# Kernel optimization log

Measured on AMD Instinct MI355X. Metric: run time of the kernel, lower is better.

## Reference

```python
import jax, jax.numpy as jnp
import numpy as np

H, DK, NW = 16, 8, 8   # num_heads, d_k (== n_wires_attn), n_wires_ffn
EPS = 1e-5


def _ln(x, g, b):
    mu = jnp.mean(x, axis=-1, keepdims=True)
    v = jnp.mean((x - mu) ** 2, axis=-1, keepdims=True)
    return (x - mu) / jnp.sqrt(v + EPS) * g + b


def setup_inputs() -> dict:
    key = jax.random.key(0)
    ks = jax.random.split(key, 10)
    B, S, E, F = 4, 1024, 128, 512

    def lin(k, o, i):
        lim = 1.0 / np.sqrt(i)
        k1, k2 = jax.random.split(k)
        W = jax.random.uniform(k1, (o, i), minval=-lim, maxval=lim, dtype=jnp.float32)
        b = jax.random.uniform(k2, (o,), minval=-lim, maxval=lim, dtype=jnp.float32)
        return W, b

    Wq, bq = lin(ks[0], E, E)
    Wk, bk = lin(ks[1], E, E)
    Wv, bv = lin(ks[2], E, E)
    Wo, bo = lin(ks[3], E, E)
    W1, b1 = lin(ks[4], F, NW)
    W2, b2 = lin(ks[5], E, F)
    rx_params = jax.random.uniform(ks[6], (H, DK), minval=0.0, maxval=2.0 * np.pi, dtype=jnp.float32)
    ry_params = jax.random.uniform(ks[7], (NW,), minval=0.0, maxval=2.0 * np.pi, dtype=jnp.float32)
    x = jax.random.normal(ks[8], (B, S, E), dtype=jnp.float32)
    return dict(x=x, Wq=Wq, bq=bq, Wk=Wk, bk=bk, Wv=Wv, bv=bv,
                rx_params=rx_params, Wo=Wo, bo=bo, ry_params=ry_params,
                W1=W1, b1=b1, W2=W2, b2=b2,
                ln1_g=jnp.ones((E,), jnp.float32), ln1_b=jnp.zeros((E,), jnp.float32),
                ln2_g=jnp.ones((E,), jnp.float32), ln2_b=jnp.zeros((E,), jnp.float32))


def reference(x, Wq, bq, Wk, bk, Wv, bv, rx_params, Wo, bo, ry_params,
              W1, b1, W2, b2, ln1_g, ln1_b, ln2_g, ln2_b):
    B, S, E = x.shape
    # q projection; k/v are computed in the original but never used downstream
    q = (x @ Wq.T + bq).reshape(B, S, H, DK).transpose(0, 2, 1, 3)  # [B,H,S,dk]
    # per-head single-qubit circuit RX(phi)RX(q)|0> -> <Z> = cos(q + phi)
    out = jnp.cos(q + rx_params[None, :, None, :])                  # [B,H,S,dk]
    scores = jnp.einsum('bhsd,bhtd->bhst', out, out) / np.sqrt(DK)  # [B,H,S,S]
    attn = jax.nn.softmax(scores, axis=-1)
    ctx = jnp.einsum('bhst,bhtd->bhsd', attn, out)
    ctx = ctx.transpose(0, 2, 1, 3).reshape(B, S, E)
    x1 = _ln(x + ctx @ Wo.T + bo, ln1_g, ln1_b)
    # FFN circuit RY(phi)RX(x)|0> -> <Z> = cos(x)*cos(phi); only first NW feats used
    qout = jnp.cos(x1[..., :NW]) * jnp.cos(ry_params)               # [B,S,NW]
    ffn = jax.nn.relu(qout @ W1.T + b1) @ W2.T + b2
    return _ln(x1 + ffn, ln2_g, ln2_b)
```

## Files before the change

### kernel.cpp

```cpp
#include <hip/hip_runtime.h>
#include <math.h>

constexpr int B_ = 4, S_ = 1024, E_ = 128, H_ = 16, DK_ = 8, F_ = 512;
constexpr int R_ = B_ * S_;
#define EPSV 1e-5f

constexpr int OFF_WQT  = 0;
constexpr int OFF_WOT  = OFF_WQT + E_ * E_;
constexpr int OFF_W2T  = OFF_WOT + E_ * E_;
constexpr int OFF_QCB  = OFF_W2T + F_ * E_;
constexpr int OFF_VTB  = OFF_QCB + 262144;
constexpr int OFF_X1   = OFF_QCB;
constexpr int OFF_CTX  = OFF_VTB + 262144;
constexpr int OFF_QOUT = OFF_CTX + R_ * E_;

typedef __attribute__((ext_vector_type(4)))  short short4v;
typedef __attribute__((ext_vector_type(16))) float f32x16;

static __device__ __forceinline__ void fma4(float4& acc, float s, const float4 v) {
    acc.x = fmaf(s, v.x, acc.x);
    acc.y = fmaf(s, v.y, acc.y);
    acc.z = fmaf(s, v.z, acc.z);
    acc.w = fmaf(s, v.w, acc.w);
}

static __device__ __forceinline__ short4v pack2(unsigned a, unsigned b) {
    union { unsigned u[2]; short4v s; } t;
    t.u[0] = a; t.u[1] = b;
    return t.s;
}

static __device__ __forceinline__ short4v cvt4_bf16(float a, float b, float c, float d) {
    unsigned p0, p1;
    asm("v_cvt_pk_bf16_f32 %0, %1, %2" : "=v"(p0) : "v"(a), "v"(b));
    asm("v_cvt_pk_bf16_f32 %0, %1, %2" : "=v"(p1) : "v"(c), "v"(d));
    return pack2(p0, p1);
}

__global__ __launch_bounds__(256) void k_transpose(const float* __restrict__ Wq,
                                                   const float* __restrict__ Wo,
                                                   const float* __restrict__ W2,
                                                   float* __restrict__ ws) {
    int idx = blockIdx.x * 256 + threadIdx.x;
    if (idx < 16384) {
        int e = idx >> 7, k = idx & 127;
        ws[OFF_WQT + k * 128 + e] = Wq[idx];
    } else if (idx < 32768) {
        int j = idx - 16384;
        int e = j >> 7, k = j & 127;
        ws[OFF_WOT + k * 128 + e] = Wo[j];
    } else if (idx < 98304) {
        int j = idx - 32768;
        int e = j >> 9, f = j & 511;
        ws[OFF_W2T + f * 128 + e] = W2[j];
    }
}

__global__ __launch_bounds__(256) void k_qproj(const float* __restrict__ x,
                                               const float* __restrict__ bq,
                                               const float* __restrict__ rx,
                                               const float* __restrict__ WqT,
                                               short* __restrict__ qcb,
                                               short* __restrict__ vtb) {
    __shared__ __attribute__((aligned(16))) float xs[8][128];
    const int tid = threadIdx.x;
    const int row0 = blockIdx.x * 8;
    ((float4*)xs)[tid] = ((const float4*)(x + row0 * E_))[tid];
    __syncthreads();
    const int cg = tid & 31, rs = tid >> 5;
    const int c0 = cg * 4;
    const float* wp = WqT + c0;
    float4 acc = {0.f, 0.f, 0.f, 0.f};
#pragma unroll 4
    for (int k0 = 0; k0 < 128; k0 += 4) {
        const float4 u  = *(const float4*)&xs[rs][k0];
        const float4 w0 = *(const float4*)(wp + (k0 + 0) * 128);
        const float4 w1 = *(const float4*)(wp + (k0 + 1) * 128);
        const float4 w2 = *(const float4*)(wp + (k0 + 2) * 128);
        const float4 w3 = *(const float4*)(wp + (k0 + 3) * 128);
        fma4(acc, u.x, w0);
        fma4(acc, u.y, w1);
        fma4(acc, u.z, w2);
        fma4(acc, u.w, w3);
    }
    const float4 bb = *(const float4*)(bq + c0);
    const float4 rr = *(const float4*)(rx + c0);
    const int gr = row0 + rs;
    const int b = gr >> 10, s = gr & 1023;
    const int h = c0 >> 3, d0 = c0 & 7;
    const int bh = b * H_ + h;
    float4 o;
    o.x = cosf(acc.x + bb.x + rr.x);
    o.y = cosf(acc.y + bb.y + rr.y);
    o.z = cosf(acc.z + bb.z + rr.z);
    o.w = cosf(acc.w + bb.w + rr.w);
    const short4v q4 = cvt4_bf16(o.x, o.y, o.z, o.w);
    *(short4v*)(qcb + (size_t)(bh * S_ + s) * 8 + d0) = q4;
    vtb[(bh * 8 + d0 + 0) * S_ + s] = q4[0];
    vtb[(bh * 8 + d0 + 1) * S_ + s] = q4[1];
    vtb[(bh * 8 + d0 + 2) * S_ + s] = q4[2];
    vtb[(bh * 8 + d0 + 3) * S_ + s] = q4[3];
}

__global__ __launch_bounds__(256) void k_attn(const short* __restrict__ qcb,
                                              const short* __restrict__ vtb,
                                              float* __restrict__ ctx) {
    constexpr float SC = 0.35355339059327373f;
    const int tid = threadIdx.x;
    const int bh = blockIdx.x >> 3;
    const int qt = blockIdx.x & 7;
    const int lane = tid & 63;
    const int row = lane & 31, hi = lane >> 5;
    const int q0 = qt * 128 + (tid >> 6) * 32;

    const short4v qfrag = *(const short4v*)(qcb + (size_t)(bh * S_ + q0 + row) * 8 + 4 * hi);
    const short* kb = qcb + (size_t)bh * S_ * 8 + 4 * hi;
    const bool vok = row < 8;
    const short* vb = vtb + (size_t)(bh * 8 + (row & 7)) * S_ + 4 * hi;
    const short4v zf = {0, 0, 0, 0};

    f32x16 pacc = {0,0,0,0,0,0,0,0,0,0,0,0,0,0,0,0};
    const f32x16 zacc = {0,0,0,0,0,0,0,0,0,0,0,0,0,0,0,0};
    float lsum = 0.f;

#pragma unroll 2
    for (int tk = 0; tk < S_; tk += 32) {
        const short4v kfrag = *(const short4v*)(kb + (size_t)(tk + row) * 8);
        f32x16 sd = __builtin_amdgcn_mfma_f32_32x32x8bf16_1k(kfrag, qfrag, zacc, 0, 0, 0);

        short4v pb0, pb1, pb2, pb3;
#define PCHUNK(c, pbv) { \
        const float e0 = __expf(sd[4*(c)+0] * SC); \
        const float e1 = __expf(sd[4*(c)+1] * SC); \
        const float e2 = __expf(sd[4*(c)+2] * SC); \
        const float e3 = __expf(sd[4*(c)+3] * SC); \
        lsum += (e0 + e1) + (e2 + e3); \
        pbv = cvt4_bf16(e0, e1, e2, e3); }
        PCHUNK(0, pb0)
        PCHUNK(1, pb1)
        PCHUNK(2, pb2)
        PCHUNK(3, pb3)
#undef PCHUNK

        const short4v v0 = vok ? *(const short4v*)(vb + tk +  0) : zf;
        const short4v v1 = vok ? *(const short4v*)(vb + tk +  8) : zf;
        const short4v v2 = vok ? *(const short4v*)(vb + tk + 16) : zf;
        const short4v v3 = vok ? *(const short4v*)(vb + tk + 24) : zf;
        pacc = __builtin_amdgcn_mfma_f32_32x32x8bf16_1k(v0, pb0, pacc, 0, 0, 0);
        pacc = __builtin_amdgcn_mfma_f32_32x32x8bf16_1k(v1, pb1, pacc, 0, 0, 0);
        pacc = __builtin_amdgcn_mfma_f32_32x32x8bf16_1k(v2, pb2, pacc, 0, 0, 0);
        pacc = __builtin_amdgcn_mfma_f32_32x32x8bf16_1k(v3, pb3, pacc, 0, 0, 0);
    }

    lsum += __shfl_xor(lsum, 32);
    const float inv = 1.0f / lsum;
    const int b = bh >> 4, h = bh & 15;
    float4 o;
    o.x = pacc[0] * inv; o.y = pacc[1] * inv;
    o.z = pacc[2] * inv; o.w = pacc[3] * inv;
    *(float4*)(ctx + (size_t)(b * S_ + q0 + row) * E_ + h * 8 + 4 * hi) = o;
}

__global__ __launch_bounds__(256) void k_oproj_ln1(const float* __restrict__ ctx,
                                                   const float* __restrict__ WoT,
                                                   const float* __restrict__ bo,
                                                   const float* __restrict__ x,
                                                   const float* __restrict__ g1,
                                                   const float* __restrict__ bln1,
                                                   const float* __restrict__ ry,
                                                   float* __restrict__ x1,
                                                   float* __restrict__ qout) {
    __shared__ __attribute__((aligned(16))) float cs[8][128];
    const int tid = threadIdx.x;
    const int row0 = blockIdx.x * 8;
    ((float4*)cs)[tid] = ((const float4*)(ctx + row0 * E_))[tid];
    __syncthreads();
    const int cg = tid & 31, rs = tid >> 5;
    const int c0 = cg * 4;
    const float* wp = WoT + c0;
    float4 acc = {0.f, 0.f, 0.f, 0.f};
#pragma unroll 4
    for (int k0 = 0; k0 < 128; k0 += 4) {
        const float4 u  = *(const float4*)&cs[rs][k0];
        const float4 w0 = *(const float4*)(wp + (k0 + 0) * 128);
        const float4 w1 = *(const float4*)(wp + (k0 + 1) * 128);
        const float4 w2 = *(const float4*)(wp + (k0 + 2) * 128);
        const float4 w3 = *(const float4*)(wp + (k0 + 3) * 128);
        fma4(acc, u.x, w0);
        fma4(acc, u.y, w1);
        fma4(acc, u.z, w2);
        fma4(acc, u.w, w3);
    }
    const int gr = row0 + rs;
    const float4 bb = *(const float4*)(bo + c0);
    const float4 xx = *(const float4*)(x + gr * E_ + c0);
    float4 y;
    y.x = acc.x + bb.x + xx.x;
    y.y = acc.y + bb.y + xx.y;
    y.z = acc.z + bb.z + xx.z;
    y.w = acc.w + bb.w + xx.w;
    float s = (y.x + y.y) + (y.z + y.w);
    float q = fmaf(y.x, y.x, y.y * y.y) + fmaf(y.z, y.z, y.w * y.w);
#pragma unroll
    for (int m = 1; m < 32; m <<= 1) {
        s += __shfl_xor(s, m);
        q += __shfl_xor(q, m);
    }
    const float mu = s * (1.0f / 128.0f);
    const float var = q * (1.0f / 128.0f) - mu * mu;
    const float is = rsqrtf(var + EPSV);
    const float4 gg = *(const float4*)(g1 + c0);
    const float4 lb = *(const float4*)(bln1 + c0);
    float4 o;
    o.x = (y.x - mu) * is * gg.x + lb.x;
    o.y = (y.y - mu) * is * gg.y + lb.y;
    o.z = (y.z - mu) * is * gg.z + lb.z;
    o.w = (y.w - mu) * is * gg.w + lb.w;
    *(float4*)(x1 + gr * E_ + c0) = o;
    if (c0 < 8) {
        float4 qo;
        qo.x = cosf(o.x) * cosf(ry[c0 + 0]);
        qo.y = cosf(o.y) * cosf(ry[c0 + 1]);
        qo.z = cosf(o.z) * cosf(ry[c0 + 2]);
        qo.w = cosf(o.w) * cosf(ry[c0 + 3]);
        *(float4*)(qout + gr * 8 + c0) = qo;
    }
}

__global__ __launch_bounds__(256) void k_ffn_ln2(const float* __restrict__ qout,
                                                 const float* __restrict__ W1,
                                                 const float* __restrict__ b1,
                                                 const float* __restrict__ W2T,
                                                 const float* __restrict__ b2,
                                                 const float* __restrict__ x1,
                                                 const float* __restrict__ g2,
                                                 const float* __restrict__ bln2,
                                                 float* __restrict__ out) {
    __shared__ __attribute__((aligned(16))) float qs[8][8];
    __shared__ __attribute__((aligned(16))) float h1[8][512];
    const int tid = threadIdx.x;
    const int row0 = blockIdx.x * 8;
    if (tid < 16) ((float4*)qs)[tid] = ((const float4*)(qout + row0 * 8))[tid];
    __syncthreads();
#pragma unroll
    for (int i = 0; i < 16; ++i) {
        const int f = ((i & 1) << 8) + tid;
        const int r = i >> 1;
        const float4 wa = *(const float4*)(W1 + f * 8);
        const float4 wb = *(const float4*)(W1 + f * 8 + 4);
        float v = b1[f];
        v = fmaf(qs[r][0], wa.x, v); v = fmaf(qs[r][1], wa.y, v);
        v = fmaf(qs[r][2], wa.z, v); v = fmaf(qs[r][3], wa.w, v);
        v = fmaf(qs[r][4], wb.x, v); v = fmaf(qs[r][5], wb.y, v);
        v = fmaf(qs[r][6], wb.z, v); v = fmaf(qs[r][7], wb.w, v);
        h1[r][f] = fmaxf(v, 0.0f);
    }
    __syncthreads();
    const int cg = tid & 31, rs = tid >> 5;
    const int c0 = cg * 4;
    const float* wp = W2T + c0;
    float4 acc = {0.f, 0.f, 0.f, 0.f};
#pragma unroll 4
    for (int f0 = 0; f0 < 512; f0 += 4) {
        const float4 u  = *(const float4*)&h1[rs][f0];
        const float4 w0 = *(const float4*)(wp + (f0 + 0) * 128);
        const float4 w1 = *(const float4*)(wp + (f0 + 1) * 128);
        const float4 w2 = *(const float4*)(wp + (f0 + 2) * 128);
        const float4 w3 = *(const float4*)(wp + (f0 + 3) * 128);
        fma4(acc, u.x, w0);
        fma4(acc, u.y, w1);
        fma4(acc, u.z, w2);
        fma4(acc, u.w, w3);
    }
    const int gr = row0 + rs;
    const float4 bb = *(const float4*)(b2 + c0);
    const float4 xx = *(const float4*)(x1 + gr * E_ + c0);
    float4 y;
    y.x = acc.x + bb.x + xx.x;
    y.y = acc.y + bb.y + xx.y;
    y.z = acc.z + bb.z + xx.z;
    y.w = acc.w + bb.w + xx.w;
    float s = (y.x + y.y) + (y.z + y.w);
    float q = fmaf(y.x, y.x, y.y * y.y) + fmaf(y.z, y.z, y.w * y.w);
#pragma unroll
    for (int m = 1; m < 32; m <<= 1) {
        s += __shfl_xor(s, m);
        q += __shfl_xor(q, m);
    }
    const float mu = s * (1.0f / 128.0f);
    const float var = q * (1.0f / 128.0f) - mu * mu;
    const float is = rsqrtf(var + EPSV);
    const float4 gg = *(const float4*)(g2 + c0);
    const float4 lb = *(const float4*)(bln2 + c0);
    float4 o;
    o.x = (y.x - mu) * is * gg.x + lb.x;
    o.y = (y.y - mu) * is * gg.y + lb.y;
    o.z = (y.z - mu) * is * gg.z + lb.z;
    o.w = (y.w - mu) * is * gg.w + lb.w;
    *(float4*)(out + gr * E_ + c0) = o;
}

extern "C" void kernel_launch(void* const* d_in, const int* in_sizes, int n_in,
                              void* d_out, int out_size, void* d_ws, size_t ws_size,
                              hipStream_t stream) {
    const float* x   = (const float*)d_in[0];
    const float* Wq  = (const float*)d_in[1];
    const float* bq  = (const float*)d_in[2];
    const float* rx  = (const float*)d_in[7];
    const float* Wo  = (const float*)d_in[8];
    const float* bo  = (const float*)d_in[9];
    const float* ry  = (const float*)d_in[10];
    const float* W1  = (const float*)d_in[11];
    const float* b1  = (const float*)d_in[12];
    const float* W2  = (const float*)d_in[13];
    const float* b2  = (const float*)d_in[14];
    const float* g1  = (const float*)d_in[15];
    const float* bl1 = (const float*)d_in[16];
    const float* g2  = (const float*)d_in[17];
    const float* bl2 = (const float*)d_in[18];
    float* ws  = (float*)d_ws;
    float* out = (float*)d_out;
    short* qcb = (short*)(ws + OFF_QCB);
    short* vtb = (short*)(ws + OFF_VTB);

    k_transpose<<<dim3(384), dim3(256), 0, stream>>>(Wq, Wo, W2, ws);
    k_qproj<<<dim3(R_ / 8), dim3(256), 0, stream>>>(x, bq, rx, ws + OFF_WQT, qcb, vtb);
    k_attn<<<dim3(B_ * H_ * 8), dim3(256), 0, stream>>>(qcb, vtb, ws + OFF_CTX);
    k_oproj_ln1<<<dim3(R_ / 8), dim3(256), 0, stream>>>(ws + OFF_CTX, ws + OFF_WOT, bo, x,
                                                        g1, bl1, ry,
                                                        ws + OFF_X1, ws + OFF_QOUT);
    k_ffn_ln2<<<dim3(R_ / 8), dim3(256), 0, stream>>>(ws + OFF_QOUT, W1, b1, ws + OFF_W2T,
                                                      b2, ws + OFF_X1, g2, bl2, out);
}
```

Baseline: 181.2 us.

## Process two rows per thread, stage V transpose in LDS, tile weight transpose

The projection, o-proj+LN1 and FFN+LN2 kernels now handle 16 rows per block, with each thread computing two rows. This reuses every weight float4 load across two accumulators and halves the block count. The q-projection stages the transposed V tile in shared memory, so vtb is written with 16-byte coalesced stores instead of scattered 2-byte stores. The weight transpose kernel uses a 32x32 padded LDS tile with float4 loads and stores. The trade-off is higher register use and fewer blocks, which could lower occupancy on a GPU this size.

```diff
diff --git a/kernel.cpp b/kernel.cpp
--- a/kernel.cpp
+++ b/kernel.cpp
@@ -15,6 +15,7 @@
 constexpr int OFF_QOUT = OFF_CTX + R_ * E_;
 
 typedef __attribute__((ext_vector_type(4)))  short short4v;
+typedef __attribute__((ext_vector_type(8)))  short short8v;
 typedef __attribute__((ext_vector_type(16))) float f32x16;
 
 static __device__ __forceinline__ void fma4(float4& acc, float s, const float4 v) {
@@ -41,19 +42,24 @@
                                                    const float* __restrict__ Wo,
                                                    const float* __restrict__ W2,
                                                    float* __restrict__ ws) {
-    int idx = blockIdx.x * 256 + threadIdx.x;
-    if (idx < 16384) {
-        int e = idx >> 7, k = idx & 127;
-        ws[OFF_WQT + k * 128 + e] = Wq[idx];
-    } else if (idx < 32768) {
-        int j = idx - 16384;
-        int e = j >> 7, k = j & 127;
-        ws[OFF_WOT + k * 128 + e] = Wo[j];
-    } else if (idx < 98304) {
-        int j = idx - 32768;
-        int e = j >> 9, f = j & 511;
-        ws[OFF_W2T + f * 128 + e] = W2[j];
-    }
+    __shared__ float ts[32][33];
+    const int t = blockIdx.x, tid = threadIdx.x;
+    const float* src; float* dst; int lds_, ldd, r0s, c0s;
+    if (t < 16)      { src = Wq; dst = ws + OFF_WQT; lds_ = 128; ldd = 128;
+                       r0s = (t & 3) * 32;        c0s = (t >> 2) * 32; }
+    else if (t < 32) { int u = t - 16; src = Wo; dst = ws + OFF_WOT; lds_ = 128; ldd = 128;
+                       r0s = (u & 3) * 32;        c0s = (u >> 2) * 32; }
+    else             { int u = t - 32; src = W2; dst = ws + OFF_W2T; lds_ = 512; ldd = 128;
+                       r0s = (u & 3) * 32;        c0s = (u >> 2) * 32; }
+    const int rr = tid >> 3, cc = (tid & 7) * 4;
+    const float4 v = *(const float4*)(src + (r0s + rr) * lds_ + c0s + cc);
+    ts[rr][cc + 0] = v.x; ts[rr][cc + 1] = v.y;
+    ts[rr][cc + 2] = v.z; ts[rr][cc + 3] = v.w;
+    __syncthreads();
+    float4 o;
+    o.x = ts[cc + 0][rr]; o.y = ts[cc + 1][rr];
+    o.z = ts[cc + 2][rr]; o.w = ts[cc + 3][rr];
+    *(float4*)(dst + (c0s + rr) * ldd + r0s + cc) = o;
 }
 
 __global__ __launch_bounds__(256) void k_qproj(const float* __restrict__ x,
@@ -62,44 +68,57 @@
                                                const float* __restrict__ WqT,
                                                short* __restrict__ qcb,
                                                short* __restrict__ vtb) {
-    __shared__ __attribute__((aligned(16))) float xs[8][128];
+    __shared__ __attribute__((aligned(16))) float xs[16][128];
+    __shared__ __attribute__((aligned(16))) short vts[128][20];
     const int tid = threadIdx.x;
-    const int row0 = blockIdx.x * 8;
-    ((float4*)xs)[tid] = ((const float4*)(x + row0 * E_))[tid];
-    __syncthreads();
-    const int cg = tid & 31, rs = tid >> 5;
-    const int c0 = cg * 4;
+    const int row0 = blockIdx.x * 16;
+    {
+        const float4* src = (const float4*)(x + row0 * E_);
+        ((float4*)xs)[tid]       = src[tid];
+        ((float4*)xs)[tid + 256] = src[tid + 256];
+    }
+    __syncthreads();
+    const int cg = tid & 31, rg = tid >> 5;
+    const int c0 = cg * 4, r0 = rg * 2;
     const float* wp = WqT + c0;
-    float4 acc = {0.f, 0.f, 0.f, 0.f};
+    float4 a0 = {0.f,0.f,0.f,0.f}, a1 = {0.f,0.f,0.f,0.f};
 #pragma unroll 4
     for (int k0 = 0; k0 < 128; k0 += 4) {
-        const float4 u  = *(const float4*)&xs[rs][k0];
         const float4 w0 = *(const float4*)(wp + (k0 + 0) * 128);
         const float4 w1 = *(const float4*)(wp + (k0 + 1) * 128);
         const float4 w2 = *(const float4*)(wp + (k0 + 2) * 128);
         const float4 w3 = *(const float4*)(wp + (k0 + 3) * 128);
-        fma4(acc, u.x, w0);
-        fma4(acc, u.y, w1);
-        fma4(acc, u.z, w2);
-        fma4(acc, u.w, w3);
+        const float4 u0 = *(const float4*)&xs[r0][k0];
+        const float4 u1 = *(const float4*)&xs[r0 + 1][k0];
+        fma4(a0, u0.x, w0); fma4(a1, u1.x, w0);
+        fma4(a0, u0.y, w1); fma4(a1, u1.y, w1);
+        fma4(a0, u0.z, w2); fma4(a1, u1.z, w2);
+        fma4(a0, u0.w, w3); fma4(a1, u1.w, w3);
     }
     const float4 bb = *(const float4*)(bq + c0);
     const float4 rr = *(const float4*)(rx + c0);
-    const int gr = row0 + rs;
-    const int b = gr >> 10, s = gr & 1023;
+    const int b = row0 >> 10, sB = row0 & 1023;
     const int h = c0 >> 3, d0 = c0 & 7;
     const int bh = b * H_ + h;
-    float4 o;
-    o.x = cosf(acc.x + bb.x + rr.x);
-    o.y = cosf(acc.y + bb.y + rr.y);
-    o.z = cosf(acc.z + bb.z + rr.z);
-    o.w = cosf(acc.w + bb.w + rr.w);
-    const short4v q4 = cvt4_bf16(o.x, o.y, o.z, o.w);
-    *(short4v*)(qcb + (size_t)(bh * S_ + s) * 8 + d0) = q4;
-    vtb[(bh * 8 + d0 + 0) * S_ + s] = q4[0];
-    vtb[(bh * 8 + d0 + 1) * S_ + s] = q4[1];
-    vtb[(bh * 8 + d0 + 2) * S_ + s] = q4[2];
-    vtb[(bh * 8 + d0 + 3) * S_ + s] = q4[3];
+    float4 o0, o1;
+    o0.x = cosf(a0.x + bb.x + rr.x); o0.y = cosf(a0.y + bb.y + rr.y);
+    o0.z = cosf(a0.z + bb.z + rr.z); o0.w = cosf(a0.w + bb.w + rr.w);
+    o1.x = cosf(a1.x + bb.x + rr.x); o1.y = cosf(a1.y + bb.y + rr.y);
+    o1.z = cosf(a1.z + bb.z + rr.z); o1.w = cosf(a1.w + bb.w + rr.w);
+    const short4v q0 = cvt4_bf16(o0.x, o0.y, o0.z, o0.w);
+    const short4v q1 = cvt4_bf16(o1.x, o1.y, o1.z, o1.w);
+    *(short4v*)(qcb + (size_t)(bh * S_ + sB + r0) * 8 + d0)     = q0;
+    *(short4v*)(qcb + (size_t)(bh * S_ + sB + r0 + 1) * 8 + d0) = q1;
+    vts[c0 + 0][r0] = q0[0]; vts[c0 + 1][r0] = q0[1];
+    vts[c0 + 2][r0] = q0[2]; vts[c0 + 3][r0] = q0[3];
+    vts[c0 + 0][r0 + 1] = q1[0]; vts[c0 + 1][r0 + 1] = q1[1];
+    vts[c0 + 2][r0 + 1] = q1[2]; vts[c0 + 3][r0 + 1] = q1[3];
+    __syncthreads();
+    const int e = tid >> 1, hf = tid & 1;
+    short8v vv;
+#pragma unroll
+    for (int j = 0; j < 8; ++j) vv[j] = vts[e][hf * 8 + j];
+    *(short8v*)(vtb + (size_t)(b * 128 + e) * S_ + sB + hf * 8) = vv;
 }
 
 __global__ __launch_bounds__(256) void k_attn(const short* __restrict__ qcb,
@@ -170,60 +189,79 @@
                                                    const float* __restrict__ ry,
                                                    float* __restrict__ x1,
                                                    float* __restrict__ qout) {
-    __shared__ __attribute__((aligned(16))) float cs[8][128];
+    __shared__ __attribute__((aligned(16))) float cs[16][128];
     const int tid = threadIdx.x;
-    const int row0 = blockIdx.x * 8;
-    ((float4*)cs)[tid] = ((const float4*)(ctx + row0 * E_))[tid];
-    __syncthreads();
-    const int cg = tid & 31, rs = tid >> 5;
-    const int c0 = cg * 4;
+    const int row0 = blockIdx.x * 16;
+    {
+        const float4* src = (const float4*)(ctx + row0 * E_);
+        ((float4*)cs)[tid]       = src[tid];
+        ((float4*)cs)[tid + 256] = src[tid + 256];
+    }
+    __syncthreads();
+    const int cg = tid & 31, rg = tid >> 5;
+    const int c0 = cg * 4, r0 = rg * 2;
     const float* wp = WoT + c0;
-    float4 acc = {0.f, 0.f, 0.f, 0.f};
+    float4 a0 = {0.f,0.f,0.f,0.f}, a1 = {0.f,0.f,0.f,0.f};
 #pragma unroll 4
     for (int k0 = 0; k0 < 128; k0 += 4) {
-        const float4 u  = *(const float4*)&cs[rs][k0];
         const float4 w0 = *(const float4*)(wp + (k0 + 0) * 128);
         const float4 w1 = *(const float4*)(wp + (k0 + 1) * 128);
         const float4 w2 = *(const float4*)(wp + (k0 + 2) * 128);
         const float4 w3 = *(const float4*)(wp + (k0 + 3) * 128);
-        fma4(acc, u.x, w0);
-        fma4(acc, u.y, w1);
-        fma4(acc, u.z, w2);
-        fma4(acc, u.w, w3);
-    }
-    const int gr = row0 + rs;
+        const float4 u0 = *(const float4*)&cs[r0][k0];
+        const float4 u1 = *(const float4*)&cs[r0 + 1][k0];
+        fma4(a0, u0.x, w0); fma4(a1, u1.x, w0);
+        fma4(a0, u0.y, w1); fma4(a1, u1.y, w1);
+        fma4(a0, u0.z, w2); fma4(a1, u1.z, w2);
+        fma4(a0, u0.w, w3); fma4(a1, u1.w, w3);
+    }
+    const int gr0 = row0 + r0, gr1 = gr0 + 1;
     const float4 bb = *(const float4*)(bo + c0);
-    const float4 xx = *(const float4*)(x + gr * E_ + c0);
-    float4 y;
-    y.x = acc.x + bb.x + xx.x;
-    y.y = acc.y + bb.y + xx.y;
-    y.z = acc.z + bb.z + xx.z;
-    y.w = acc.w + bb.w + xx.w;
-    float s = (y.x + y.y) + (y.z + y.w);
-    float q = fmaf(y.x, y.x, y.y * y.y) + fmaf(y.z, y.z, y.w * y.w);
+    const float4 xa = *(const float4*)(x + gr0 * E_ + c0);
+    const float4 xb = *(const float4*)(x + gr1 * E_ + c0);
+    float4 y0, y1;
+    y0.x = a0.x + bb.x + xa.x; y0.y = a0.y + bb.y + xa.y;
+    y0.z = a0.z + bb.z + xa.z; y0.w = a0.w + bb.w + xa.w;
+    y1.x = a1.x + bb.x + xb.x; y1.y = a1.y + bb.y + xb.y;
+    y1.z = a1.z + bb.z + xb.z; y1.w = a1.w + bb.w + xb.w;
+    float s0 = (y0.x + y0.y) + (y0.z + y0.w);
+    float q0 = fmaf(y0.x, y0.x, y0.y * y0.y) + fmaf(y0.z, y0.z, y0.w * y0.w);
+    float s1 = (y1.x + y1.y) + (y1.z + y1.w);
+    float q1 = fmaf(y1.x, y1.x, y1.y * y1.y) + fmaf(y1.z, y1.z, y1.w * y1.w);
 #pragma unroll
     for (int m = 1; m < 32; m <<= 1) {
-        s += __shfl_xor(s, m);
-        q += __shfl_xor(q, m);
-    }
-    const float mu = s * (1.0f / 128.0f);
-    const float var = q * (1.0f / 128.0f) - mu * mu;
-    const float is = rsqrtf(var + EPSV);
+        s0 += __shfl_xor(s0, m); q0 += __shfl_xor(q0, m);
+        s1 += __shfl_xor(s1, m); q1 += __shfl_xor(q1, m);
+    }
+    const float mu0 = s0 * (1.0f / 128.0f);
+    const float is0 = rsqrtf(q0 * (1.0f / 128.0f) - mu0 * mu0 + EPSV);
+    const float mu1 = s1 * (1.0f / 128.0f);
+    const float is1 = rsqrtf(q1 * (1.0f / 128.0f) - mu1 * mu1 + EPSV);
     const float4 gg = *(const float4*)(g1 + c0);
     const float4 lb = *(const float4*)(bln1 + c0);
-    float4 o;
-    o.x = (y.x - mu) * is * gg.x + lb.x;
-    o.y = (y.y - mu) * is * gg.y + lb.y;
-    o.z = (y.z - mu) * is * gg.z + lb.z;
-    o.w = (y.w - mu) * is * gg.w + lb.w;
-    *(float4*)(x1 + gr * E_ + c0) = o;
+    float4 o0, o1;
+    o0.x = (y0.x - mu0) * is0 * gg.x + lb.x;
+    o0.y = (y0.y - mu0) * is0 * gg.y + lb.y;
+    o0.z = (y0.z - mu0) * is0 * gg.z + lb.z;
+    o0.w = (y0.w - mu0) * is0 * gg.w + lb.w;
+    o1.x = (y1.x - mu1) * is1 * gg.x + lb.x;
+    o1.y = (y1.y - mu1) * is1 * gg.y + lb.y;
+    o1.z = (y1.z - mu1) * is1 * gg.z + lb.z;
+    o1.w = (y1.w - mu1) * is1 * gg.w + lb.w;
+    *(float4*)(x1 + gr0 * E_ + c0) = o0;
+    *(float4*)(x1 + gr1 * E_ + c0) = o1;
     if (c0 < 8) {
-        float4 qo;
-        qo.x = cosf(o.x) * cosf(ry[c0 + 0]);
-        qo.y = cosf(o.y) * cosf(ry[c0 + 1]);
-        qo.z = cosf(o.z) * cosf(ry[c0 + 2]);
-        qo.w = cosf(o.w) * cosf(ry[c0 + 3]);
-        *(float4*)(qout + gr * 8 + c0) = qo;
+        float4 qo0, qo1;
+        qo0.x = cosf(o0.x) * cosf(ry[c0 + 0]);
+        qo0.y = cosf(o0.y) * cosf(ry[c0 + 1]);
+        qo0.z = cosf(o0.z) * cosf(ry[c0 + 2]);
+        qo0.w = cosf(o0.w) * cosf(ry[c0 + 3]);
+        qo1.x = cosf(o1.x) * cosf(ry[c0 + 0]);
+        qo1.y = cosf(o1.y) * cosf(ry[c0 + 1]);
+        qo1.z = cosf(o1.z) * cosf(ry[c0 + 2]);
+        qo1.w = cosf(o1.w) * cosf(ry[c0 + 3]);
+        *(float4*)(qout + gr0 * 8 + c0) = qo0;
+        *(float4*)(qout + gr1 * 8 + c0) = qo1;
     }
 }
 
@@ -236,14 +274,14 @@
                                                  const float* __restrict__ g2,
                                                  const float* __restrict__ bln2,
                                                  float* __restrict__ out) {
-    __shared__ __attribute__((aligned(16))) float qs[8][8];
-    __shared__ __attribute__((aligned(16))) float h1[8][512];
+    __shared__ __attribute__((aligned(16))) float qs[16][8];
+    __shared__ __attribute__((aligned(16))) float h1[16][512];
     const int tid = threadIdx.x;
-    const int row0 = blockIdx.x * 8;
-    if (tid < 16) ((float4*)qs)[tid] = ((const float4*)(qout + row0 * 8))[tid];
+    const int row0 = blockIdx.x * 16;
+    if (tid < 32) ((float4*)qs)[tid] = ((const float4*)(qout + row0 * 8))[tid];
     __syncthreads();
 #pragma unroll
-    for (int i = 0; i < 16; ++i) {
+    for (int i = 0; i < 32; ++i) {
         const int f = ((i & 1) << 8) + tid;
         const int r = i >> 1;
         const float4 wa = *(const float4*)(W1 + f * 8);
@@ -256,48 +294,58 @@
         h1[r][f] = fmaxf(v, 0.0f);
     }
     __syncthreads();
-    const int cg = tid & 31, rs = tid >> 5;
-    const int c0 = cg * 4;
+    const int cg = tid & 31, rg = tid >> 5;
+    const int c0 = cg * 4, r0 = rg * 2;
     const float* wp = W2T + c0;
-    float4 acc = {0.f, 0.f, 0.f, 0.f};
+    float4 a0 = {0.f,0.f,0.f,0.f}, a1 = {0.f,0.f,0.f,0.f};
 #pragma unroll 4
     for (int f0 = 0; f0 < 512; f0 += 4) {
-        const float4 u  = *(const float4*)&h1[rs][f0];
         const float4 w0 = *(const float4*)(wp + (f0 + 0) * 128);
         const float4 w1 = *(const float4*)(wp + (f0 + 1) * 128);
         const float4 w2 = *(const float4*)(wp + (f0 + 2) * 128);
         const float4 w3 = *(const float4*)(wp + (f0 + 3) * 128);
-        fma4(acc, u.x, w0);
-        fma4(acc, u.y, w1);
-        fma4(acc, u.z, w2);
-        fma4(acc, u.w, w3);
-    }
-    const int gr = row0 + rs;
+        const float4 u0 = *(const float4*)&h1[r0][f0];
+        const float4 u1 = *(const float4*)&h1[r0 + 1][f0];
+        fma4(a0, u0.x, w0); fma4(a1, u1.x, w0);
+        fma4(a0, u0.y, w1); fma4(a1, u1.y, w1);
+        fma4(a0, u0.z, w2); fma4(a1, u1.z, w2);
+        fma4(a0, u0.w, w3); fma4(a1, u1.w, w3);
+    }
+    const int gr0 = row0 + r0, gr1 = gr0 + 1;
     const float4 bb = *(const float4*)(b2 + c0);
-    const float4 xx = *(const float4*)(x1 + gr * E_ + c0);
-    float4 y;
-    y.x = acc.x + bb.x + xx.x;
-    y.y = acc.y + bb.y + xx.y;
-    y.z = acc.z + bb.z + xx.z;
-    y.w = acc.w + bb.w + xx.w;
-    float s = (y.x + y.y) + (y.z + y.w);
-    float q = fmaf(y.x, y.x, y.y * y.y) + fmaf(y.z, y.z, y.w * y.w);
+    const float4 xa = *(const float4*)(x1 + gr0 * E_ + c0);
+    const float4 xb = *(const float4*)(x1 + gr1 * E_ + c0);
+    float4 y0, y1;
+    y0.x = a0.x + bb.x + xa.x; y0.y = a0.y + bb.y + xa.y;
+    y0.z = a0.z + bb.z + xa.z; y0.w = a0.w + bb.w + xa.w;
+    y1.x = a1.x + bb.x + xb.x; y1.y = a1.y + bb.y + xb.y;
+    y1.z = a1.z + bb.z + xb.z; y1.w = a1.w + bb.w + xb.w;
+    float s0 = (y0.x + y0.y) + (y0.z + y0.w);
+    float q0 = fmaf(y0.x, y0.x, y0.y * y0.y) + fmaf(y0.z, y0.z, y0.w * y0.w);
+    float s1 = (y1.x + y1.y) + (y1.z + y1.w);
+    float q1 = fmaf(y1.x, y1.x, y1.y * y1.y) + fmaf(y1.z, y1.z, y1.w * y1.w);
 #pragma unroll
     for (int m = 1; m < 32; m <<= 1) {
-        s += __shfl_xor(s, m);
-        q += __shfl_xor(q, m);
-    }
-    const float mu = s * (1.0f / 128.0f);
-    const float var = q * (1.0f / 128.0f) - mu * mu;
-    const float is = rsqrtf(var + EPSV);
+        s0 += __shfl_xor(s0, m); q0 += __shfl_xor(q0, m);
+        s1 += __shfl_xor(s1, m); q1 += __shfl_xor(q1, m);
+    }
+    const float mu0 = s0 * (1.0f / 128.0f);
+    const float is0 = rsqrtf(q0 * (1.0f / 128.0f) - mu0 * mu0 + EPSV);
+    const float mu1 = s1 * (1.0f / 128.0f);
+    const float is1 = rsqrtf(q1 * (1.0f / 128.0f) - mu1 * mu1 + EPSV);
     const float4 gg = *(const float4*)(g2 + c0);
     const float4 lb = *(const float4*)(bln2 + c0);
-    float4 o;
-    o.x = (y.x - mu) * is * gg.x + lb.x;
-    o.y = (y.y - mu) * is * gg.y + lb.y;
-    o.z = (y.z - mu) * is * gg.z + lb.z;
-    o.w = (y.w - mu) * is * gg.w + lb.w;
-    *(float4*)(out + gr * E_ + c0) = o;
+    float4 o0, o1;
+    o0.x = (y0.x - mu0) * is0 * gg.x + lb.x;
+    o0.y = (y0.y - mu0) * is0 * gg.y + lb.y;
+    o0.z = (y0.z - mu0) * is0 * gg.z + lb.z;
+    o0.w = (y0.w - mu0) * is0 * gg.w + lb.w;
+    o1.x = (y1.x - mu1) * is1 * gg.x + lb.x;
+    o1.y = (y1.y - mu1) * is1 * gg.y + lb.y;
+    o1.z = (y1.z - mu1) * is1 * gg.z + lb.z;
+    o1.w = (y1.w - mu1) * is1 * gg.w + lb.w;
+    *(float4*)(out + gr0 * E_ + c0) = o0;
+    *(float4*)(out + gr1 * E_ + c0) = o1;
 }
 
 extern "C" void kernel_launch(void* const* d_in, const int* in_sizes, int n_in,
@@ -323,12 +371,12 @@
     short* qcb = (short*)(ws + OFF_QCB);
     short* vtb = (short*)(ws + OFF_VTB);
 
-    k_transpose<<<dim3(384), dim3(256), 0, stream>>>(Wq, Wo, W2, ws);
-    k_qproj<<<dim3(R_ / 8), dim3(256), 0, stream>>>(x, bq, rx, ws + OFF_WQT, qcb, vtb);
+    k_transpose<<<dim3(96), dim3(256), 0, stream>>>(Wq, Wo, W2, ws);
+    k_qproj<<<dim3(R_ / 16), dim3(256), 0, stream>>>(x, bq, rx, ws + OFF_WQT, qcb, vtb);
     k_attn<<<dim3(B_ * H_ * 8), dim3(256), 0, stream>>>(qcb, vtb, ws + OFF_CTX);
-    k_oproj_ln1<<<dim3(R_ / 8), dim3(256), 0, stream>>>(ws + OFF_CTX, ws + OFF_WOT, bo, x,
-                                                        g1, bl1, ry,
-                                                        ws + OFF_X1, ws + OFF_QOUT);
-    k_ffn_ln2<<<dim3(R_ / 8), dim3(256), 0, stream>>>(ws + OFF_QOUT, W1, b1, ws + OFF_W2T,
-                                                      b2, ws + OFF_X1, g2, bl2, out);
-}
+    k_oproj_ln1<<<dim3(R_ / 16), dim3(256), 0, stream>>>(ws + OFF_CTX, ws + OFF_WOT, bo, x,
+                                                         g1, bl1, ry,
+                                                         ws + OFF_X1, ws + OFF_QOUT);
+    k_ffn_ln2<<<dim3(R_ / 16), dim3(256), 0, stream>>>(ws + OFF_QOUT, W1, b1, ws + OFF_W2T,
+                                                       b2, ws + OFF_X1, g2, bl2, out);
+}
```

After: 188.4 us. 4.0% more time.

## Move projections and FFN GEMMs to bf16 MFMA with bf16 intermediates

Applied to the files above, without the earlier changes.

Replaces the scalar fp32 FMA GEMMs in the q-projection, output projection and FFN kernels with 32x32x8 bf16 MFMA tiles over 32-row blocks. A new prep kernel converts x and the weights to bf16 instead of transposing them. Intermediates (ctx, x1, qout) are now stored as bf16, and LayerNorm is redone through a shared-memory transpose. This cuts FMA work and memory traffic at the cost of lower precision in the residual x1 and the GEMM inputs.

```diff
diff --git a/kernel.cpp b/kernel.cpp
--- a/kernel.cpp
+++ b/kernel.cpp
@@ -5,24 +5,20 @@
 constexpr int R_ = B_ * S_;
 #define EPSV 1e-5f
 
-constexpr int OFF_WQT  = 0;
-constexpr int OFF_WOT  = OFF_WQT + E_ * E_;
-constexpr int OFF_W2T  = OFF_WOT + E_ * E_;
-constexpr int OFF_QCB  = OFF_W2T + F_ * E_;
-constexpr int OFF_VTB  = OFF_QCB + 262144;
-constexpr int OFF_X1   = OFF_QCB;
-constexpr int OFF_CTX  = OFF_VTB + 262144;
-constexpr int OFF_QOUT = OFF_CTX + R_ * E_;
+constexpr size_t OFF_XB   = 0;
+constexpr size_t OFF_WQB  = OFF_XB   + 524288;
+constexpr size_t OFF_WOB  = OFF_WQB  + 16384;
+constexpr size_t OFF_W1B  = OFF_WOB  + 16384;
+constexpr size_t OFF_W2B  = OFF_W1B  + 4096;
+constexpr size_t OFF_QCB  = OFF_W2B  + 65536;
+constexpr size_t OFF_VTB  = OFF_QCB  + 524288;
+constexpr size_t OFF_CTXB = OFF_VTB  + 524288;
+constexpr size_t OFF_X1B  = OFF_CTXB + 524288;
+constexpr size_t OFF_QOB  = OFF_X1B  + 524288;
 
 typedef __attribute__((ext_vector_type(4)))  short short4v;
+typedef __attribute__((ext_vector_type(8)))  short short8v;
 typedef __attribute__((ext_vector_type(16))) float f32x16;
-
-static __device__ __forceinline__ void fma4(float4& acc, float s, const float4 v) {
-    acc.x = fmaf(s, v.x, acc.x);
-    acc.y = fmaf(s, v.y, acc.y);
-    acc.z = fmaf(s, v.z, acc.z);
-    acc.w = fmaf(s, v.w, acc.w);
-}
 
 static __device__ __forceinline__ short4v pack2(unsigned a, unsigned b) {
     union { unsigned u[2]; short4v s; } t;
@@ -37,74 +33,79 @@
     return pack2(p0, p1);
 }
 
-__global__ __launch_bounds__(256) void k_transpose(const float* __restrict__ Wq,
-                                                   const float* __restrict__ Wo,
-                                                   const float* __restrict__ W2,
-                                                   float* __restrict__ ws) {
-    int idx = blockIdx.x * 256 + threadIdx.x;
-    if (idx < 16384) {
-        int e = idx >> 7, k = idx & 127;
-        ws[OFF_WQT + k * 128 + e] = Wq[idx];
-    } else if (idx < 32768) {
-        int j = idx - 16384;
-        int e = j >> 7, k = j & 127;
-        ws[OFF_WOT + k * 128 + e] = Wo[j];
-    } else if (idx < 98304) {
-        int j = idx - 32768;
-        int e = j >> 9, f = j & 511;
-        ws[OFF_W2T + f * 128 + e] = W2[j];
-    }
-}
-
-__global__ __launch_bounds__(256) void k_qproj(const float* __restrict__ x,
+static __device__ __forceinline__ short8v cvt8_bf16(const float* v) {
+    const short4v a = cvt4_bf16(v[0], v[1], v[2], v[3]);
+    const short4v b = cvt4_bf16(v[4], v[5], v[6], v[7]);
+    short8v r;
+    r[0]=a[0]; r[1]=a[1]; r[2]=a[2]; r[3]=a[3];
+    r[4]=b[0]; r[5]=b[1]; r[6]=b[2]; r[7]=b[3];
+    return r;
+}
+
+static __device__ __forceinline__ float b2f(short v) {
+    return __uint_as_float(((unsigned)(unsigned short)v) << 16);
+}
+
+__global__ __launch_bounds__(256) void k_prep(const float* __restrict__ x,
+                                              const float* __restrict__ Wq,
+                                              const float* __restrict__ Wo,
+                                              const float* __restrict__ W1,
+                                              const float* __restrict__ W2,
+                                              short* __restrict__ ws) {
+    const int idx = blockIdx.x * 256 + threadIdx.x;
+    const float* src; short* dst; int local;
+    if (idx < 131072)      { src = x;  dst = ws + OFF_XB;  local = idx; }
+    else if (idx < 135168) { src = Wq; dst = ws + OFF_WQB; local = idx - 131072; }
+    else if (idx < 139264) { src = Wo; dst = ws + OFF_WOB; local = idx - 135168; }
+    else if (idx < 140288) { src = W1; dst = ws + OFF_W1B; local = idx - 139264; }
+    else                   { src = W2; dst = ws + OFF_W2B; local = idx - 140288; }
+    const float4 v = ((const float4*)src)[local];
+    ((short4v*)dst)[local] = cvt4_bf16(v.x, v.y, v.z, v.w);
+}
+
+__global__ __launch_bounds__(256) void k_qproj(const short* __restrict__ xb,
                                                const float* __restrict__ bq,
                                                const float* __restrict__ rx,
-                                               const float* __restrict__ WqT,
+                                               const short* __restrict__ wqb,
                                                short* __restrict__ qcb,
                                                short* __restrict__ vtb) {
-    __shared__ __attribute__((aligned(16))) float xs[8][128];
-    const int tid = threadIdx.x;
-    const int row0 = blockIdx.x * 8;
-    ((float4*)xs)[tid] = ((const float4*)(x + row0 * E_))[tid];
-    __syncthreads();
-    const int cg = tid & 31, rs = tid >> 5;
-    const int c0 = cg * 4;
-    const float* wp = WqT + c0;
-    float4 acc = {0.f, 0.f, 0.f, 0.f};
-#pragma unroll 4
-    for (int k0 = 0; k0 < 128; k0 += 4) {
-        const float4 u  = *(const float4*)&xs[rs][k0];
-        const float4 w0 = *(const float4*)(wp + (k0 + 0) * 128);
-        const float4 w1 = *(const float4*)(wp + (k0 + 1) * 128);
-        const float4 w2 = *(const float4*)(wp + (k0 + 2) * 128);
-        const float4 w3 = *(const float4*)(wp + (k0 + 3) * 128);
-        fma4(acc, u.x, w0);
-        fma4(acc, u.y, w1);
-        fma4(acc, u.z, w2);
-        fma4(acc, u.w, w3);
-    }
-    const float4 bb = *(const float4*)(bq + c0);
-    const float4 rr = *(const float4*)(rx + c0);
-    const int gr = row0 + rs;
-    const int b = gr >> 10, s = gr & 1023;
-    const int h = c0 >> 3, d0 = c0 & 7;
+    const int tid = threadIdx.x, lane = tid & 63, w = tid >> 6;
+    const int row = lane & 31, hi = lane >> 5;
+    const int r0 = blockIdx.x * 32;
+    const int c  = w * 32 + row;
+    const short* ap = xb  + (size_t)(r0 + row) * 128 + 4 * hi;
+    const short* bp = wqb + (size_t)c * 128 + 4 * hi;
+    f32x16 acc = {0,0,0,0,0,0,0,0,0,0,0,0,0,0,0,0};
+#pragma unroll
+    for (int k0 = 0; k0 < 128; k0 += 8) {
+        const short4v af = *(const short4v*)(ap + k0);
+        const short4v bf = *(const short4v*)(bp + k0);
+        acc = __builtin_amdgcn_mfma_f32_32x32x8bf16_1k(af, bf, acc, 0, 0, 0);
+    }
+    const float add = bq[c] + rx[c];
+    float cv[16];
+#pragma unroll
+    for (int i = 0; i < 16; ++i) cv[i] = cosf(acc[i] + add);
+    const int b = r0 >> 10, sloc0 = r0 & 1023;
+    const int h = c >> 3, d = c & 7;
     const int bh = b * H_ + h;
-    float4 o;
-    o.x = cosf(acc.x + bb.x + rr.x);
-    o.y = cosf(acc.y + bb.y + rr.y);
-    o.z = cosf(acc.z + bb.z + rr.z);
-    o.w = cosf(acc.w + bb.w + rr.w);
-    const short4v q4 = cvt4_bf16(o.x, o.y, o.z, o.w);
-    *(short4v*)(qcb + (size_t)(bh * S_ + s) * 8 + d0) = q4;
-    vtb[(bh * 8 + d0 + 0) * S_ + s] = q4[0];
-    vtb[(bh * 8 + d0 + 1) * S_ + s] = q4[1];
-    vtb[(bh * 8 + d0 + 2) * S_ + s] = q4[2];
-    vtb[(bh * 8 + d0 + 3) * S_ + s] = q4[3];
+    short* qbase = qcb + ((size_t)bh * 1024 + sloc0) * 8 + d;
+    short* vbase = vtb + ((size_t)bh * 8 + d) * 1024 + sloc0;
+#pragma unroll
+    for (int rq = 0; rq < 4; ++rq) {
+        const short4v v = cvt4_bf16(cv[4*rq+0], cv[4*rq+1], cv[4*rq+2], cv[4*rq+3]);
+        const int sb = 8 * rq + 4 * hi;
+        *(short4v*)(vbase + sb) = v;
+        qbase[(sb + 0) * 8] = v[0];
+        qbase[(sb + 1) * 8] = v[1];
+        qbase[(sb + 2) * 8] = v[2];
+        qbase[(sb + 3) * 8] = v[3];
+    }
 }
 
 __global__ __launch_bounds__(256) void k_attn(const short* __restrict__ qcb,
                                               const short* __restrict__ vtb,
-                                              float* __restrict__ ctx) {
+                                              short* __restrict__ ctxb) {
     constexpr float SC = 0.35355339059327373f;
     const int tid = threadIdx.x;
     const int bh = blockIdx.x >> 3;
@@ -155,149 +156,148 @@
     lsum += __shfl_xor(lsum, 32);
     const float inv = 1.0f / lsum;
     const int b = bh >> 4, h = bh & 15;
-    float4 o;
-    o.x = pacc[0] * inv; o.y = pacc[1] * inv;
-    o.z = pacc[2] * inv; o.w = pacc[3] * inv;
-    *(float4*)(ctx + (size_t)(b * S_ + q0 + row) * E_ + h * 8 + 4 * hi) = o;
-}
-
-__global__ __launch_bounds__(256) void k_oproj_ln1(const float* __restrict__ ctx,
-                                                   const float* __restrict__ WoT,
+    const short4v co = cvt4_bf16(pacc[0] * inv, pacc[1] * inv,
+                                 pacc[2] * inv, pacc[3] * inv);
+    *(short4v*)(ctxb + (size_t)(b * S_ + q0 + row) * 128 + h * 8 + 4 * hi) = co;
+}
+
+__global__ __launch_bounds__(256) void k_oproj_ln1(const short* __restrict__ ctxb,
+                                                   const short* __restrict__ wob,
                                                    const float* __restrict__ bo,
                                                    const float* __restrict__ x,
                                                    const float* __restrict__ g1,
                                                    const float* __restrict__ bln1,
                                                    const float* __restrict__ ry,
-                                                   float* __restrict__ x1,
-                                                   float* __restrict__ qout) {
-    __shared__ __attribute__((aligned(16))) float cs[8][128];
-    const int tid = threadIdx.x;
-    const int row0 = blockIdx.x * 8;
-    ((float4*)cs)[tid] = ((const float4*)(ctx + row0 * E_))[tid];
+                                                   short* __restrict__ x1b,
+                                                   short* __restrict__ qob) {
+    __shared__ float yt[32][129];
+    const int tid = threadIdx.x, lane = tid & 63, w = tid >> 6;
+    const int row = lane & 31, hi = lane >> 5;
+    const int r0 = blockIdx.x * 32;
+    const int c  = w * 32 + row;
+    const short* ap = ctxb + (size_t)(r0 + row) * 128 + 4 * hi;
+    const short* bp = wob  + (size_t)c * 128 + 4 * hi;
+    f32x16 acc = {0,0,0,0,0,0,0,0,0,0,0,0,0,0,0,0};
+#pragma unroll
+    for (int k0 = 0; k0 < 128; k0 += 8) {
+        const short4v af = *(const short4v*)(ap + k0);
+        const short4v bf = *(const short4v*)(bp + k0);
+        acc = __builtin_amdgcn_mfma_f32_32x32x8bf16_1k(af, bf, acc, 0, 0, 0);
+    }
+    const float bov = bo[c];
+#pragma unroll
+    for (int i = 0; i < 16; ++i) {
+        const int sl = (i & 3) + 8 * (i >> 2) + 4 * hi;
+        yt[sl][c] = acc[i] + bov + x[(size_t)(r0 + sl) * 128 + c];
+    }
     __syncthreads();
-    const int cg = tid & 31, rs = tid >> 5;
-    const int c0 = cg * 4;
-    const float* wp = WoT + c0;
-    float4 acc = {0.f, 0.f, 0.f, 0.f};
-#pragma unroll 4
-    for (int k0 = 0; k0 < 128; k0 += 4) {
-        const float4 u  = *(const float4*)&cs[rs][k0];
-        const float4 w0 = *(const float4*)(wp + (k0 + 0) * 128);
-        const float4 w1 = *(const float4*)(wp + (k0 + 1) * 128);
-        const float4 w2 = *(const float4*)(wp + (k0 + 2) * 128);
-        const float4 w3 = *(const float4*)(wp + (k0 + 3) * 128);
-        fma4(acc, u.x, w0);
-        fma4(acc, u.y, w1);
-        fma4(acc, u.z, w2);
-        fma4(acc, u.w, w3);
-    }
-    const int gr = row0 + rs;
-    const float4 bb = *(const float4*)(bo + c0);
-    const float4 xx = *(const float4*)(x + gr * E_ + c0);
-    float4 y;
-    y.x = acc.x + bb.x + xx.x;
-    y.y = acc.y + bb.y + xx.y;
-    y.z = acc.z + bb.z + xx.z;
-    y.w = acc.w + bb.w + xx.w;
-    float s = (y.x + y.y) + (y.z + y.w);
-    float q = fmaf(y.x, y.x, y.y * y.y) + fmaf(y.z, y.z, y.w * y.w);
-#pragma unroll
-    for (int m = 1; m < 32; m <<= 1) {
+    const int rr = tid >> 3, cl = (tid & 7) * 16;
+    float yv[16], s = 0.f, q = 0.f;
+#pragma unroll
+    for (int j = 0; j < 16; ++j) {
+        const float v = yt[rr][cl + j];
+        yv[j] = v; s += v; q = fmaf(v, v, q);
+    }
+#pragma unroll
+    for (int m = 1; m < 8; m <<= 1) {
         s += __shfl_xor(s, m);
         q += __shfl_xor(q, m);
     }
     const float mu = s * (1.0f / 128.0f);
-    const float var = q * (1.0f / 128.0f) - mu * mu;
-    const float is = rsqrtf(var + EPSV);
-    const float4 gg = *(const float4*)(g1 + c0);
-    const float4 lb = *(const float4*)(bln1 + c0);
-    float4 o;
-    o.x = (y.x - mu) * is * gg.x + lb.x;
-    o.y = (y.y - mu) * is * gg.y + lb.y;
-    o.z = (y.z - mu) * is * gg.z + lb.z;
-    o.w = (y.w - mu) * is * gg.w + lb.w;
-    *(float4*)(x1 + gr * E_ + c0) = o;
-    if (c0 < 8) {
-        float4 qo;
-        qo.x = cosf(o.x) * cosf(ry[c0 + 0]);
-        qo.y = cosf(o.y) * cosf(ry[c0 + 1]);
-        qo.z = cosf(o.z) * cosf(ry[c0 + 2]);
-        qo.w = cosf(o.w) * cosf(ry[c0 + 3]);
-        *(float4*)(qout + gr * 8 + c0) = qo;
-    }
-}
-
-__global__ __launch_bounds__(256) void k_ffn_ln2(const float* __restrict__ qout,
-                                                 const float* __restrict__ W1,
+    const float is = rsqrtf(q * (1.0f / 128.0f) - mu * mu + EPSV);
+    float ov[16];
+#pragma unroll
+    for (int j = 0; j < 16; ++j)
+        ov[j] = (yv[j] - mu) * is * g1[cl + j] + bln1[cl + j];
+    *(short8v*)(x1b + (size_t)(r0 + rr) * 128 + cl)     = cvt8_bf16(ov);
+    *(short8v*)(x1b + (size_t)(r0 + rr) * 128 + cl + 8) = cvt8_bf16(ov + 8);
+    if (cl == 0) {
+        float qo[8];
+#pragma unroll
+        for (int j = 0; j < 8; ++j) qo[j] = cosf(ov[j]) * cosf(ry[j]);
+        *(short8v*)(qob + (size_t)(r0 + rr) * 8) = cvt8_bf16(qo);
+    }
+}
+
+__global__ __launch_bounds__(256) void k_ffn_ln2(const short* __restrict__ qob,
+                                                 const short* __restrict__ w1b,
                                                  const float* __restrict__ b1,
-                                                 const float* __restrict__ W2T,
+                                                 const short* __restrict__ w2b,
                                                  const float* __restrict__ b2,
-                                                 const float* __restrict__ x1,
+                                                 const short* __restrict__ x1b,
                                                  const float* __restrict__ g2,
                                                  const float* __restrict__ bln2,
                                                  float* __restrict__ out) {
-    __shared__ __attribute__((aligned(16))) float qs[8][8];
-    __shared__ __attribute__((aligned(16))) float h1[8][512];
-    const int tid = threadIdx.x;
-    const int row0 = blockIdx.x * 8;
-    if (tid < 16) ((float4*)qs)[tid] = ((const float4*)(qout + row0 * 8))[tid];
+    __shared__ short h1b[32][516];
+    __shared__ float yt[32][129];
+    const int tid = threadIdx.x, lane = tid & 63, w = tid >> 6;
+    const int row = lane & 31, hi = lane >> 5;
+    const int r0 = blockIdx.x * 32;
+    const f32x16 zacc = {0,0,0,0,0,0,0,0,0,0,0,0,0,0,0,0};
+
+    const short4v af1 = *(const short4v*)(qob + (size_t)(r0 + row) * 8 + 4 * hi);
+#pragma unroll
+    for (int it = 0; it < 4; ++it) {
+        const int f = it * 128 + w * 32 + row;
+        const short4v bf1 = *(const short4v*)(w1b + (size_t)f * 8 + 4 * hi);
+        f32x16 a1 = __builtin_amdgcn_mfma_f32_32x32x8bf16_1k(af1, bf1, zacc, 0, 0, 0);
+        const float bv = b1[f];
+#pragma unroll
+        for (int rq = 0; rq < 4; ++rq) {
+            const short4v hv = cvt4_bf16(fmaxf(a1[4*rq+0] + bv, 0.f),
+                                         fmaxf(a1[4*rq+1] + bv, 0.f),
+                                         fmaxf(a1[4*rq+2] + bv, 0.f),
+                                         fmaxf(a1[4*rq+3] + bv, 0.f));
+            const int sb = 8 * rq + 4 * hi;
+            h1b[sb + 0][f] = hv[0];
+            h1b[sb + 1][f] = hv[1];
+            h1b[sb + 2][f] = hv[2];
+            h1b[sb + 3][f] = hv[3];
+        }
+    }
     __syncthreads();
+
+    const int c = w * 32 + row;
+    const short* ap2 = &h1b[row][4 * hi];
+    const short* bp2 = w2b + (size_t)c * 512 + 4 * hi;
+    f32x16 acc = zacc;
+#pragma unroll 8
+    for (int k0 = 0; k0 < 512; k0 += 8) {
+        const short4v af = *(const short4v*)(ap2 + k0);
+        const short4v bf = *(const short4v*)(bp2 + k0);
+        acc = __builtin_amdgcn_mfma_f32_32x32x8bf16_1k(af, bf, acc, 0, 0, 0);
+    }
+    const float b2v = b2[c];
 #pragma unroll
     for (int i = 0; i < 16; ++i) {
-        const int f = ((i & 1) << 8) + tid;
-        const int r = i >> 1;
-        const float4 wa = *(const float4*)(W1 + f * 8);
-        const float4 wb = *(const float4*)(W1 + f * 8 + 4);
-        float v = b1[f];
-        v = fmaf(qs[r][0], wa.x, v); v = fmaf(qs[r][1], wa.y, v);
-        v = fmaf(qs[r][2], wa.z, v); v = fmaf(qs[r][3], wa.w, v);
-        v = fmaf(qs[r][4], wb.x, v); v = fmaf(qs[r][5], wb.y, v);
-        v = fmaf(qs[r][6], wb.z, v); v = fmaf(qs[r][7], wb.w, v);
-        h1[r][f] = fmaxf(v, 0.0f);
+        const int sl = (i & 3) + 8 * (i >> 2) + 4 * hi;
+        yt[sl][c] = acc[i] + b2v + b2f(x1b[(size_t)(r0 + sl) * 128 + c]);
     }
     __syncthreads();
-    const int cg = tid & 31, rs = tid >> 5;
-    const int c0 = cg * 4;
-    const float* wp = W2T + c0;
-    float4 acc = {0.f, 0.f, 0.f, 0.f};
-#pragma unroll 4
-    for (int f0 = 0; f0 < 512; f0 += 4) {
-        const float4 u  = *(const float4*)&h1[rs][f0];
-        const float4 w0 = *(const float4*)(wp + (f0 + 0) * 128);
-        const float4 w1 = *(const float4*)(wp + (f0 + 1) * 128);
-        const float4 w2 = *(const float4*)(wp + (f0 + 2) * 128);
-        const float4 w3 = *(const float4*)(wp + (f0 + 3) * 128);
-        fma4(acc, u.x, w0);
-        fma4(acc, u.y, w1);
-        fma4(acc, u.z, w2);
-        fma4(acc, u.w, w3);
-    }
-    const int gr = row0 + rs;
-    const float4 bb = *(const float4*)(b2 + c0);
-    const float4 xx = *(const float4*)(x1 + gr * E_ + c0);
-    float4 y;
-    y.x = acc.x + bb.x + xx.x;
-    y.y = acc.y + bb.y + xx.y;
-    y.z = acc.z + bb.z + xx.z;
-    y.w = acc.w + bb.w + xx.w;
-    float s = (y.x + y.y) + (y.z + y.w);
-    float q = fmaf(y.x, y.x, y.y * y.y) + fmaf(y.z, y.z, y.w * y.w);
-#pragma unroll
-    for (int m = 1; m < 32; m <<= 1) {
+    const int rr = tid >> 3, cl = (tid & 7) * 16;
+    float yv[16], s = 0.f, q = 0.f;
+#pragma unroll
+    for (int j = 0; j < 16; ++j) {
+        const float v = yt[rr][cl + j];
+        yv[j] = v; s += v; q = fmaf(v, v, q);
+    }
+#pragma unroll
+    for (int m = 1; m < 8; m <<= 1) {
         s += __shfl_xor(s, m);
         q += __shfl_xor(q, m);
     }
     const float mu = s * (1.0f / 128.0f);
-    const float var = q * (1.0f / 128.0f) - mu * mu;
-    const float is = rsqrtf(var + EPSV);
-    const float4 gg = *(const float4*)(g2 + c0);
-    const float4 lb = *(const float4*)(bln2 + c0);
-    float4 o;
-    o.x = (y.x - mu) * is * gg.x + lb.x;
-    o.y = (y.y - mu) * is * gg.y + lb.y;
-    o.z = (y.z - mu) * is * gg.z + lb.z;
-    o.w = (y.w - mu) * is * gg.w + lb.w;
-    *(float4*)(out + gr * E_ + c0) = o;
+    const float is = rsqrtf(q * (1.0f / 128.0f) - mu * mu + EPSV);
+    float* op = out + (size_t)(r0 + rr) * 128 + cl;
+#pragma unroll
+    for (int jj = 0; jj < 4; ++jj) {
+        float4 o;
+        o.x = (yv[4*jj+0] - mu) * is * g2[cl + 4*jj + 0] + bln2[cl + 4*jj + 0];
+        o.y = (yv[4*jj+1] - mu) * is * g2[cl + 4*jj + 1] + bln2[cl + 4*jj + 1];
+        o.z = (yv[4*jj+2] - mu) * is * g2[cl + 4*jj + 2] + bln2[cl + 4*jj + 2];
+        o.w = (yv[4*jj+3] - mu) * is * g2[cl + 4*jj + 3] + bln2[cl + 4*jj + 3];
+        *(float4*)(op + 4 * jj) = o;
+    }
 }
 
 extern "C" void kernel_launch(void* const* d_in, const int* in_sizes, int n_in,
@@ -318,17 +318,18 @@
     const float* bl1 = (const float*)d_in[16];
     const float* g2  = (const float*)d_in[17];
     const float* bl2 = (const float*)d_in[18];
-    float* ws  = (float*)d_ws;
+    short* ws  = (short*)d_ws;
     float* out = (float*)d_out;
-    short* qcb = (short*)(ws + OFF_QCB);
-    short* vtb = (short*)(ws + OFF_VTB);
-
-    k_transpose<<<dim3(384), dim3(256), 0, stream>>>(Wq, Wo, W2, ws);
-    k_qproj<<<dim3(R_ / 8), dim3(256), 0, stream>>>(x, bq, rx, ws + OFF_WQT, qcb, vtb);
-    k_attn<<<dim3(B_ * H_ * 8), dim3(256), 0, stream>>>(qcb, vtb, ws + OFF_CTX);
-    k_oproj_ln1<<<dim3(R_ / 8), dim3(256), 0, stream>>>(ws + OFF_CTX, ws + OFF_WOT, bo, x,
-                                                        g1, bl1, ry,
-                                                        ws + OFF_X1, ws + OFF_QOUT);
-    k_ffn_ln2<<<dim3(R_ / 8), dim3(256), 0, stream>>>(ws + OFF_QOUT, W1, b1, ws + OFF_W2T,
-                                                      b2, ws + OFF_X1, g2, bl2, out);
-}
+
+    k_prep<<<dim3(612), dim3(256), 0, stream>>>(x, Wq, Wo, W1, W2, ws);
+    k_qproj<<<dim3(R_ / 32), dim3(256), 0, stream>>>(ws + OFF_XB, bq, rx, ws + OFF_WQB,
+                                                     ws + OFF_QCB, ws + OFF_VTB);
+    k_attn<<<dim3(B_ * H_ * 8), dim3(256), 0, stream>>>(ws + OFF_QCB, ws + OFF_VTB,
+                                                        ws + OFF_CTXB);
+    k_oproj_ln1<<<dim3(R_ / 32), dim3(256), 0, stream>>>(ws + OFF_CTXB, ws + OFF_WOB, bo, x,
+                                                         g1, bl1, ry,
+                                                         ws + OFF_X1B, ws + OFF_QOB);
+    k_ffn_ln2<<<dim3(R_ / 32), dim3(256), 0, stream>>>(ws + OFF_QOB, ws + OFF_W1B, b1,
+                                                       ws + OFF_W2B, b2, ws + OFF_X1B,
+                                                       g2, bl2, out);
+}
```

Result: faster. 154.7 us (-14.6%).
